# Kernel tuning notes

Hardware: AMD Instinct MI355X
Metric: run time of the kernel (lower is better)

Reference implementation:

```python
import jax, jax.numpy as jnp
import numpy as np

P = 3            # spline degree
N_KNOTS = 68     # len(t); K = N_KNOTS - P - 1 = 64
B, D_IN, D_OUT = 4096, 256, 256


def bspline_basis(u, t, p):
    """Vectorized Cox-de Boor recursion.
    u: (N,) evaluation points; t: (n,) sorted knot vector.
    Returns (N, n - p - 1) basis matrix.
    """
    n = t.shape[0]
    uu = u[:, None]                                   # (N, 1)
    # degree-0 indicators over half-open knot intervals: (N, n-1)
    Bmat = ((uu >= t[None, :-1]) & (uu < t[None, 1:])).astype(u.dtype)
    for d in range(1, p + 1):
        ld = t[d:n - 1] - t[:n - d - 1]               # (n-d-1,) left denominators
        rd = t[d + 1:] - t[1:n - d]                   # (n-d-1,) right denominators
        lt = jnp.where(ld > 0, (uu - t[None, :n - d - 1]) / jnp.where(ld > 0, ld, 1.0), 0.0)
        rt = jnp.where(rd > 0, (t[None, d + 1:] - uu) / jnp.where(rd > 0, rd, 1.0), 0.0)
        Bmat = lt * Bmat[:, :-1] + rt * Bmat[:, 1:]
    return Bmat                                        # (N, K)


def setup_inputs() -> dict:
    key = jax.random.key(0)
    k1, k2 = jax.random.split(key)
    K = N_KNOTS - P - 1
    x = jax.random.normal(k1, (B, D_IN), dtype=jnp.float32)
    coeffs = 0.01 * jax.random.normal(k2, (D_OUT, D_IN, K), dtype=jnp.float32)
    mask = jnp.ones((D_OUT, D_IN), dtype=jnp.float32)
    t = jnp.linspace(-4.0, 4.0, N_KNOTS, dtype=jnp.float32)
    return {"x": x, "coeffs": coeffs, "mask": mask, "t": t}


def reference(x, coeffs, mask, t):
    b, d_in = x.shape
    # basis for all (batch, input-dim) points at once -> (B, d_in, K)
    Bx = bspline_basis(x.reshape(-1), t, P).reshape(b, d_in, -1)
    C = coeffs * mask[..., None]                      # (d_out, d_in, K)
    y = jnp.einsum('bik,oik->bo', Bx, C)              # (B, d_out)
    return y
```

## Files before the change

### kernel.cpp

```cpp
#include <hip/hip_runtime.h>

#define NKNOTS 68
#define B_     4096
#define DIN    256
#define DOUT   256
#define KB_    64
#define BM     128
#define BN     128
#define LDT    72
#define KSPLIT 16
#define IPS    (DIN / KSPLIT)

typedef unsigned short ushort_t;
typedef __bf16 bf16_t;
typedef bf16_t  bf16x8   __attribute__((ext_vector_type(8)));
typedef float   f32x4    __attribute__((ext_vector_type(4)));
typedef unsigned int u32x4 __attribute__((ext_vector_type(4)));
typedef ushort_t us16x4  __attribute__((ext_vector_type(4)));

typedef __attribute__((address_space(1))) const unsigned int gu32;
typedef __attribute__((address_space(3))) unsigned int lu32;

__device__ __forceinline__ float bf2f(ushort_t b) {
    union { unsigned u; float f; } c; c.u = ((unsigned)b) << 16; return c.f;
}
__device__ __forceinline__ ushort_t f2bf(float f) {
    union { float f; unsigned u; } c; c.f = f;
    unsigned u = c.u;
    return (ushort_t)((u + 0x7FFFu + ((u >> 16) & 1u)) >> 16);
}
__device__ __forceinline__ bool is_fp32(const void* tkn) {
    return ((*(const unsigned*)tkn) & 0xFFFFu) == 0u;
}

__global__ void kan_prep(const void* __restrict__ coeffs,
                         const void* __restrict__ mask,
                         const void* __restrict__ x,
                         const void* __restrict__ tkn,
                         ushort_t* __restrict__ cp,
                         ushort_t* __restrict__ basis4,
                         unsigned char* __restrict__ span) {
    __shared__ float tt[NKNOTS];
    int blk = blockIdx.x;
    int lt  = threadIdx.x;
    bool f32 = is_fp32(tkn);

    if (blk < 2048) {
        int tid = blk * 256 + lt;
        int oi = tid >> 3;
        int k8 = (tid & 7) * 8;
        size_t base = (size_t)oi * KB_ + k8;
        float v[8], m;
        if (f32) {
            const float* cf = (const float*)coeffs + base;
            f32x4 a = *(const f32x4*)cf;
            f32x4 b = *(const f32x4*)(cf + 4);
            v[0]=a.x; v[1]=a.y; v[2]=a.z; v[3]=a.w; v[4]=b.x; v[5]=b.y; v[6]=b.z; v[7]=b.w;
            m = ((const float*)mask)[oi];
        } else {
            const ushort_t* ch = (const ushort_t*)coeffs + base;
            u32x4 w = *(const u32x4*)ch;
            const ushort_t* h = (const ushort_t*)&w;
            #pragma unroll
            for (int e = 0; e < 8; ++e) v[e] = bf2f(h[e]);
            m = bf2f(((const ushort_t*)mask)[oi]);
        }
        us16x4 o0v, o1v;
        #pragma unroll
        for (int e = 0; e < 4; ++e) o0v[e] = f2bf(v[e] * m);
        #pragma unroll
        for (int e = 0; e < 4; ++e) o1v[e] = f2bf(v[4 + e] * m);
        *(us16x4*)(cp + base)     = o0v;
        *(us16x4*)(cp + base + 4) = o1v;
    } else {
        if (lt < NKNOTS) tt[lt] = f32 ? ((const float*)tkn)[lt] : bf2f(((const ushort_t*)tkn)[lt]);
        __syncthreads();
        int g = (blk - 2048) * 256 + lt;
        float u = f32 ? ((const float*)x)[g] : bf2f(((const ushort_t*)x)[g]);
        float N0 = 0.f, N1 = 0.f, N2 = 0.f, N3 = 0.f;
        int j = 0;
        bool valid = (u >= tt[0]) && (u < tt[NKNOTS - 1]);
        if (valid) {
            int lo = 0, hi = NKNOTS - 1;
            #pragma unroll
            for (int it = 0; it < 7; ++it) {
                int mid = (lo + hi) >> 1;
                if (u < tt[mid]) hi = mid; else lo = mid;
            }
            j = lo;
            float Nv[4];
            Nv[0] = 1.f; Nv[1] = 0.f; Nv[2] = 0.f; Nv[3] = 0.f;
            #pragma unroll
            for (int d = 1; d <= 3; ++d) {
                float saved = 0.f;
                #pragma unroll
                for (int r = 0; r < 3; ++r) {
                    if (r < d) {
                        int il = j + r + 1 - d;
                        int ir = j + r + 1;
                        il = il < 0 ? 0 : (il > 67 ? 67 : il);
                        ir = ir > 67 ? 67 : ir;
                        float tl = tt[il], tr = tt[ir];
                        float denom = tr - tl;
                        float temp = (denom > 0.f) ? Nv[r] / denom : 0.f;
                        Nv[r] = saved + (tr - u) * temp;
                        saved = (u - tl) * temp;
                    }
                }
                Nv[d] = saved;
            }
            N0 = Nv[0]; N1 = Nv[1]; N2 = Nv[2]; N3 = Nv[3];
        }
        int s = j - 3;
        int sc = s < 0 ? 0 : (s > 60 ? 60 : s);
        us16x4 o4;
        #pragma unroll
        for (int r = 0; r < 4; ++r) {
            int rr = (sc + r) - s;
            float v = 0.f;
            v = (rr == 0) ? N0 : v;
            v = (rr == 1) ? N1 : v;
            v = (rr == 2) ? N2 : v;
            v = (rr == 3) ? N3 : v;
            o4[r] = f2bf(v);
        }
        ((us16x4*)basis4)[g] = o4;
        span[g] = (unsigned char)sc;
    }
}

__global__ __launch_bounds__(256, 4) void kan_gemm(
    const ushort_t* __restrict__ cp,
    const ushort_t* __restrict__ basis4,
    const unsigned char* __restrict__ span,
    ushort_t* __restrict__ part)
{
    __shared__ __align__(16) ushort_t As[BM * LDT];
    __shared__ __align__(16) ushort_t Bs[BM * KB_];

    int t  = threadIdx.x;
    int bx = blockIdx.x;
    int kt = bx & (KSPLIT - 1);
    int mt = (bx >> 4) & 31;
    int nt = bx >> 9;
    int b0 = mt * BM;
    int o0 = nt * BN;
    int i0 = kt * IPS;

    int wave = t >> 6;
    int lane = t & 63;
    int wm = (wave & 1) * 64;
    int wn = (wave >> 1) * 64;
    int l15 = lane & 15;
    int l4  = lane >> 4;

    {
        unsigned* As32 = (unsigned*)As;
        #pragma unroll
        for (int j = 0; j < (BM * LDT / 2) / 256; ++j) As32[t + j * 256] = 0u;
    }
    __syncthreads();

    f32x4 acc[4][4];
    #pragma unroll
    for (int a = 0; a < 4; ++a)
        #pragma unroll
        for (int b = 0; b < 4; ++b)
            acc[a][b] = (f32x4){0.f, 0.f, 0.f, 0.f};

    int zrow = t >> 2;
    int zq   = t & 3;
    int last0 = 0, last1 = 0;

    for (int ii = 0; ii < IPS; ++ii) {
        int i = i0 + ii;
        size_t gi0 = (size_t)(b0 + zrow) * DIN + i;
        size_t gi1 = (size_t)(b0 + zrow + 64) * DIN + i;
        int s0 = span[gi0];
        int s1 = span[gi1];
        ushort_t bv0 = basis4[gi0 * 4 + zq];
        ushort_t bv1 = basis4[gi1 * 4 + zq];
        #pragma unroll
        for (int j = 0; j < 4; ++j) {
            int slot = wave * 256 + j * 64 + lane;
            int row  = slot >> 3;
            int c    = (slot & 7) ^ (row & 7);
            const ushort_t* g = cp + ((size_t)(o0 + row) * DIN + i) * KB_ + c * 8;
            lu32* l = (lu32*)(Bs + (wave * 256 + j * 64) * 8);
            __builtin_amdgcn_global_load_lds((gu32*)g, l, 16, 0, 0);
        }
        As[zrow * LDT + last0 + zq] = 0;
        As[(zrow + 64) * LDT + last1 + zq] = 0;
        As[zrow * LDT + s0 + zq] = bv0;
        As[(zrow + 64) * LDT + s1 + zq] = bv1;
        last0 = s0; last1 = s1;
        __syncthreads();
        #pragma unroll
        for (int ks = 0; ks < 2; ++ks) {
            bf16x8 af[4], bfr[4];
            #pragma unroll
            for (int a = 0; a < 4; ++a)
                af[a] = *(const bf16x8*)(As + (wm + a * 16 + l15) * LDT + ks * 32 + l4 * 8);
            #pragma unroll
            for (int b = 0; b < 4; ++b) {
                int brow = wn + b * 16 + l15;
                int c2 = (ks * 4 + l4) ^ (brow & 7);
                bfr[b] = *(const bf16x8*)(Bs + brow * KB_ + c2 * 8);
            }
            #pragma unroll
            for (int a = 0; a < 4; ++a)
                #pragma unroll
                for (int b = 0; b < 4; ++b)
                    acc[a][b] = __builtin_amdgcn_mfma_f32_16x16x32_bf16(af[a], bfr[b], acc[a][b], 0, 0, 0);
        }
        __syncthreads();
    }
    ushort_t* pout = part + (size_t)kt * (B_ * DOUT);
    #pragma unroll
    for (int a = 0; a < 4; ++a) {
        int row_base = b0 + wm + a * 16 + l4 * 4;
        #pragma unroll
        for (int b = 0; b < 4; ++b) {
            int col = o0 + wn + b * 16 + l15;
            #pragma unroll
            for (int e = 0; e < 4; ++e)
                pout[(size_t)(row_base + e) * DOUT + col] = f2bf(acc[a][b][e]);
        }
    }
}

__global__ void kan_reduce(const ushort_t* __restrict__ part,
                           const void* __restrict__ tkn,
                           void* __restrict__ out) {
    int g = blockIdx.x * 256 + threadIdx.x;
    const us16x4* p4 = (const us16x4*)part;
    f32x4 s = (f32x4){0.f, 0.f, 0.f, 0.f};
    #pragma unroll
    for (int kt = 0; kt < KSPLIT; ++kt) {
        us16x4 v = p4[(size_t)kt * (B_ * DOUT / 4) + g];
        s.x += bf2f(v[0]); s.y += bf2f(v[1]); s.z += bf2f(v[2]); s.w += bf2f(v[3]);
    }
    if (is_fp32(tkn)) {
        ((f32x4*)out)[g] = s;
    } else {
        us16x4 o;
        o[0] = f2bf(s.x); o[1] = f2bf(s.y); o[2] = f2bf(s.z); o[3] = f2bf(s.w);
        ((us16x4*)out)[g] = o;
    }
}

extern "C" void kernel_launch(void* const* d_in, const int* in_sizes, int n_in,
                              void* d_out, int out_size, void* d_ws, size_t ws_size,
                              hipStream_t stream) {
    const void* x      = d_in[0];
    const void* coeffs = d_in[1];
    const void* mask   = d_in[2];
    const void* tkn    = d_in[3];

    char* ws = (char*)d_ws;
    ushort_t* cp            = (ushort_t*)(ws);
    ushort_t* basis4        = (ushort_t*)(ws + (8u  << 20));
    unsigned char* spanbuf  = (unsigned char*)(ws + (16u << 20));
    ushort_t* part          = (ushort_t*)(ws + (17u << 20));

    kan_prep<<<6144, 256, 0, stream>>>(coeffs, mask, x, tkn, cp, basis4, spanbuf);
    kan_gemm<<<1024, 256, 0, stream>>>(cp, basis4, spanbuf, part);
    kan_reduce<<<1024, 256, 0, stream>>>(part, tkn, d_out);
}
```

Measured before the change: 118.6 us.

## Double-buffer coefficient tiles in LDS and prefetch next basis slice

```diff
diff --git a/kernel.cpp b/kernel.cpp
--- a/kernel.cpp
+++ b/kernel.cpp
@@ -129,14 +129,14 @@
     }
 }
 
-__global__ __launch_bounds__(256, 4) void kan_gemm(
+__global__ __launch_bounds__(256, 3) void kan_gemm(
     const ushort_t* __restrict__ cp,
     const ushort_t* __restrict__ basis4,
     const unsigned char* __restrict__ span,
     ushort_t* __restrict__ part)
 {
     __shared__ __align__(16) ushort_t As[BM * LDT];
-    __shared__ __align__(16) ushort_t Bs[BM * KB_];
+    __shared__ __align__(16) ushort_t Bs[2][BM * KB_];
 
     int t  = threadIdx.x;
     int bx = blockIdx.x;
@@ -154,12 +154,31 @@
     int l15 = lane & 15;
     int l4  = lane >> 4;
 
+    int slot0 = wave * 256 + lane;
+    int zrow = t >> 2;
+    int zq   = t & 3;
+
     {
         unsigned* As32 = (unsigned*)As;
         #pragma unroll
         for (int j = 0; j < (BM * LDT / 2) / 256; ++j) As32[t + j * 256] = 0u;
     }
-    __syncthreads();
+
+    #pragma unroll
+    for (int j = 0; j < 4; ++j) {
+        int slot = slot0 + j * 64;
+        int row  = slot >> 3;
+        int c    = (slot & 7) ^ (row & 7);
+        const ushort_t* g = cp + ((size_t)(o0 + row) * DIN + i0) * KB_ + c * 8;
+        lu32* l = (lu32*)(Bs[0] + (wave * 256 + j * 64) * 8);
+        __builtin_amdgcn_global_load_lds((gu32*)g, l, 16, 0, 0);
+    }
+    size_t gi0 = (size_t)(b0 + zrow) * DIN + i0;
+    size_t gi1 = (size_t)(b0 + zrow + 64) * DIN + i0;
+    int cur_s0 = span[gi0];
+    int cur_s1 = span[gi1];
+    ushort_t cur_b0 = basis4[gi0 * 4 + zq];
+    ushort_t cur_b1 = basis4[gi1 * 4 + zq];
 
     f32x4 acc[4][4];
     #pragma unroll
@@ -168,33 +187,35 @@
         for (int b = 0; b < 4; ++b)
             acc[a][b] = (f32x4){0.f, 0.f, 0.f, 0.f};
 
-    int zrow = t >> 2;
-    int zq   = t & 3;
+    __syncthreads();
+
     int last0 = 0, last1 = 0;
-
     for (int ii = 0; ii < IPS; ++ii) {
-        int i = i0 + ii;
-        size_t gi0 = (size_t)(b0 + zrow) * DIN + i;
-        size_t gi1 = (size_t)(b0 + zrow + 64) * DIN + i;
-        int s0 = span[gi0];
-        int s1 = span[gi1];
-        ushort_t bv0 = basis4[gi0 * 4 + zq];
-        ushort_t bv1 = basis4[gi1 * 4 + zq];
-        #pragma unroll
-        for (int j = 0; j < 4; ++j) {
-            int slot = wave * 256 + j * 64 + lane;
-            int row  = slot >> 3;
-            int c    = (slot & 7) ^ (row & 7);
-            const ushort_t* g = cp + ((size_t)(o0 + row) * DIN + i) * KB_ + c * 8;
-            lu32* l = (lu32*)(Bs + (wave * 256 + j * 64) * 8);
-            __builtin_amdgcn_global_load_lds((gu32*)g, l, 16, 0, 0);
-        }
+        int p = ii & 1;
         As[zrow * LDT + last0 + zq] = 0;
         As[(zrow + 64) * LDT + last1 + zq] = 0;
-        As[zrow * LDT + s0 + zq] = bv0;
-        As[(zrow + 64) * LDT + s1 + zq] = bv1;
-        last0 = s0; last1 = s1;
+        As[zrow * LDT + cur_s0 + zq] = cur_b0;
+        As[(zrow + 64) * LDT + cur_s1 + zq] = cur_b1;
+        last0 = cur_s0; last1 = cur_s1;
         __syncthreads();
+        if (ii + 1 < IPS) {
+            int i1 = i0 + ii + 1;
+            #pragma unroll
+            for (int j = 0; j < 4; ++j) {
+                int slot = slot0 + j * 64;
+                int row  = slot >> 3;
+                int c    = (slot & 7) ^ (row & 7);
+                const ushort_t* g = cp + ((size_t)(o0 + row) * DIN + i1) * KB_ + c * 8;
+                lu32* l = (lu32*)(Bs[p ^ 1] + (wave * 256 + j * 64) * 8);
+                __builtin_amdgcn_global_load_lds((gu32*)g, l, 16, 0, 0);
+            }
+            size_t ni0 = (size_t)(b0 + zrow) * DIN + i1;
+            size_t ni1 = (size_t)(b0 + zrow + 64) * DIN + i1;
+            cur_s0 = span[ni0];
+            cur_s1 = span[ni1];
+            cur_b0 = basis4[ni0 * 4 + zq];
+            cur_b1 = basis4[ni1 * 4 + zq];
+        }
         #pragma unroll
         for (int ks = 0; ks < 2; ++ks) {
             bf16x8 af[4], bfr[4];
@@ -205,7 +226,7 @@
             for (int b = 0; b < 4; ++b) {
                 int brow = wn + b * 16 + l15;
                 int c2 = (ks * 4 + l4) ^ (brow & 7);
-                bfr[b] = *(const bf16x8*)(Bs + brow * KB_ + c2 * 8);
+                bfr[b] = *(const bf16x8*)(Bs[p] + brow * KB_ + c2 * 8);
             }
             #pragma unroll
             for (int a = 0; a < 4; ++a)
```

Result: slower. 125.6 us (+5.9%).

## Build sparse basis MFMA fragments in registers and double-buffer coefficient tiles

Applied to the files above, without the earlier changes.

```diff
diff --git a/kernel.cpp b/kernel.cpp
--- a/kernel.cpp
+++ b/kernel.cpp
@@ -7,8 +7,7 @@
 #define KB_    64
 #define BM     128
 #define BN     128
-#define LDT    72
-#define KSPLIT 16
+#define KSPLIT 8
 #define IPS    (DIN / KSPLIT)
 
 typedef unsigned short ushort_t;
@@ -17,6 +16,7 @@
 typedef float   f32x4    __attribute__((ext_vector_type(4)));
 typedef unsigned int u32x4 __attribute__((ext_vector_type(4)));
 typedef ushort_t us16x4  __attribute__((ext_vector_type(4)));
+typedef unsigned long long u64_t;
 
 typedef __attribute__((address_space(1))) const unsigned int gu32;
 typedef __attribute__((address_space(3))) unsigned int lu32;
@@ -38,8 +38,7 @@
                          const void* __restrict__ x,
                          const void* __restrict__ tkn,
                          ushort_t* __restrict__ cp,
-                         ushort_t* __restrict__ basis4,
-                         unsigned char* __restrict__ span) {
+                         u32x4* __restrict__ rec) {
     __shared__ float tt[NKNOTS];
     int blk = blockIdx.x;
     int lt  = threadIdx.x;
@@ -113,7 +112,7 @@
         }
         int s = j - 3;
         int sc = s < 0 ? 0 : (s > 60 ? 60 : s);
-        us16x4 o4;
+        ushort_t hb[4];
         #pragma unroll
         for (int r = 0; r < 4; ++r) {
             int rr = (sc + r) - s;
@@ -122,27 +121,47 @@
             v = (rr == 1) ? N1 : v;
             v = (rr == 2) ? N2 : v;
             v = (rr == 3) ? N3 : v;
-            o4[r] = f2bf(v);
-        }
-        ((us16x4*)basis4)[g] = o4;
-        span[g] = (unsigned char)sc;
-    }
-}
-
-__global__ __launch_bounds__(256, 4) void kan_gemm(
+            hb[r] = f2bf(v);
+        }
+        u32x4 rv;
+        rv.x = ((unsigned)hb[1] << 16) | hb[0];
+        rv.y = ((unsigned)hb[3] << 16) | hb[2];
+        rv.z = (unsigned)sc;
+        rv.w = 0u;
+        rec[g] = rv;
+    }
+}
+
+__device__ __forceinline__ void build_frags(u64_t Bv, int s, int k0,
+                                            bf16x8& af0, bf16x8& af1) {
+    int e0 = s - k0;
+    bool in0 = (unsigned)(e0 + 3)  <= 10u;
+    bool in1 = (unsigned)(e0 - 29) <= 10u;
+    int e = in1 ? (e0 - 32) : e0;
+    int shm = (e << 4) & 63;
+    u64_t l = Bv << shm;
+    u64_t r = (Bv >> 1) >> (63 - shm);
+    u64_t neg = Bv >> (((-e) << 4) & 63);
+    u64_t w0 = (e >= 0) ? ((e <= 3) ? l : 0ull) : neg;
+    u64_t w1 = ((unsigned)(e - 1) <= 2u) ? r : (((unsigned)(e - 4) <= 3u) ? l : 0ull);
+    union U { u64_t q[2]; bf16x8 v; } u0, u1;
+    u0.q[0] = in0 ? w0 : 0ull; u0.q[1] = in0 ? w1 : 0ull;
+    u1.q[0] = in1 ? w0 : 0ull; u1.q[1] = in1 ? w1 : 0ull;
+    af0 = u0.v; af1 = u1.v;
+}
+
+__global__ __launch_bounds__(256, 2) void kan_gemm(
     const ushort_t* __restrict__ cp,
-    const ushort_t* __restrict__ basis4,
-    const unsigned char* __restrict__ span,
+    const u32x4* __restrict__ rec,
     ushort_t* __restrict__ part)
 {
-    __shared__ __align__(16) ushort_t As[BM * LDT];
-    __shared__ __align__(16) ushort_t Bs[BM * KB_];
+    __shared__ __align__(16) ushort_t Bs[2][BN * KB_];
 
     int t  = threadIdx.x;
     int bx = blockIdx.x;
     int kt = bx & (KSPLIT - 1);
-    int mt = (bx >> 4) & 31;
-    int nt = bx >> 9;
+    int mt = (bx >> 3) & 31;
+    int nt = bx >> 8;
     int b0 = mt * BM;
     int o0 = nt * BN;
     int i0 = kt * IPS;
@@ -153,13 +172,30 @@
     int wn = (wave >> 1) * 64;
     int l15 = lane & 15;
     int l4  = lane >> 4;
-
-    {
-        unsigned* As32 = (unsigned*)As;
-        #pragma unroll
-        for (int j = 0; j < (BM * LDT / 2) / 256; ++j) As32[t + j * 256] = 0u;
-    }
-    __syncthreads();
+    int k0  = l4 * 8;
+
+    #define STAGE(i_, p_)                                                              \
+        {                                                                              \
+            _Pragma("unroll")                                                          \
+            for (int j = 0; j < 4; ++j) {                                              \
+                int slot = wave * 256 + j * 64 + lane;                                 \
+                int row  = slot >> 3;                                                  \
+                int c    = (slot & 7) ^ (row & 7);                                     \
+                const ushort_t* g = cp + ((size_t)(o0 + row) * DIN + (i_)) * KB_ + c * 8; \
+                lu32* l = (lu32*)(&Bs[p_][(wave * 256 + j * 64) * 8]);                 \
+                __builtin_amdgcn_global_load_lds((gu32*)g, l, 16, 0, 0);               \
+            }                                                                          \
+        }
+
+    size_t ridx[4];
+    #pragma unroll
+    for (int a = 0; a < 4; ++a)
+        ridx[a] = (size_t)(b0 + wm + a * 16 + l15) * DIN + i0;
+
+    STAGE(i0, 0);
+    u32x4 rcur[4], rnext[4];
+    #pragma unroll
+    for (int a = 0; a < 4; ++a) rcur[a] = rec[ridx[a]];
 
     f32x4 acc[4][4];
     #pragma unroll
@@ -168,53 +204,42 @@
         for (int b = 0; b < 4; ++b)
             acc[a][b] = (f32x4){0.f, 0.f, 0.f, 0.f};
 
-    int zrow = t >> 2;
-    int zq   = t & 3;
-    int last0 = 0, last1 = 0;
+    __syncthreads();
 
     for (int ii = 0; ii < IPS; ++ii) {
-        int i = i0 + ii;
-        size_t gi0 = (size_t)(b0 + zrow) * DIN + i;
-        size_t gi1 = (size_t)(b0 + zrow + 64) * DIN + i;
-        int s0 = span[gi0];
-        int s1 = span[gi1];
-        ushort_t bv0 = basis4[gi0 * 4 + zq];
-        ushort_t bv1 = basis4[gi1 * 4 + zq];
-        #pragma unroll
-        for (int j = 0; j < 4; ++j) {
-            int slot = wave * 256 + j * 64 + lane;
-            int row  = slot >> 3;
-            int c    = (slot & 7) ^ (row & 7);
-            const ushort_t* g = cp + ((size_t)(o0 + row) * DIN + i) * KB_ + c * 8;
-            lu32* l = (lu32*)(Bs + (wave * 256 + j * 64) * 8);
-            __builtin_amdgcn_global_load_lds((gu32*)g, l, 16, 0, 0);
-        }
-        As[zrow * LDT + last0 + zq] = 0;
-        As[(zrow + 64) * LDT + last1 + zq] = 0;
-        As[zrow * LDT + s0 + zq] = bv0;
-        As[(zrow + 64) * LDT + s1 + zq] = bv1;
-        last0 = s0; last1 = s1;
-        __syncthreads();
-        #pragma unroll
-        for (int ks = 0; ks < 2; ++ks) {
-            bf16x8 af[4], bfr[4];
-            #pragma unroll
-            for (int a = 0; a < 4; ++a)
-                af[a] = *(const bf16x8*)(As + (wm + a * 16 + l15) * LDT + ks * 32 + l4 * 8);
+        int p = ii & 1;
+        if (ii + 1 < IPS) {
+            STAGE(i0 + ii + 1, p ^ 1);
+            #pragma unroll
+            for (int a = 0; a < 4; ++a) rnext[a] = rec[ridx[a] + ii + 1];
+        }
+        bf16x8 bfr[2][4];
+        #pragma unroll
+        for (int ks = 0; ks < 2; ++ks)
             #pragma unroll
             for (int b = 0; b < 4; ++b) {
                 int brow = wn + b * 16 + l15;
                 int c2 = (ks * 4 + l4) ^ (brow & 7);
-                bfr[b] = *(const bf16x8*)(Bs + brow * KB_ + c2 * 8);
+                bfr[ks][b] = *(const bf16x8*)(&Bs[p][brow * KB_ + c2 * 8]);
             }
-            #pragma unroll
-            for (int a = 0; a < 4; ++a)
-                #pragma unroll
-                for (int b = 0; b < 4; ++b)
-                    acc[a][b] = __builtin_amdgcn_mfma_f32_16x16x32_bf16(af[a], bfr[b], acc[a][b], 0, 0, 0);
-        }
+        #pragma unroll
+        for (int a = 0; a < 4; ++a) {
+            u64_t Bv = ((u64_t)rcur[a].y << 32) | rcur[a].x;
+            int s = (int)rcur[a].z;
+            bf16x8 af0, af1;
+            build_frags(Bv, s, k0, af0, af1);
+            #pragma unroll
+            for (int b = 0; b < 4; ++b)
+                acc[a][b] = __builtin_amdgcn_mfma_f32_16x16x32_bf16(af0, bfr[0][b], acc[a][b], 0, 0, 0);
+            #pragma unroll
+            for (int b = 0; b < 4; ++b)
+                acc[a][b] = __builtin_amdgcn_mfma_f32_16x16x32_bf16(af1, bfr[1][b], acc[a][b], 0, 0, 0);
+        }
+        #pragma unroll
+        for (int a = 0; a < 4; ++a) rcur[a] = rnext[a];
         __syncthreads();
     }
+
     ushort_t* pout = part + (size_t)kt * (B_ * DOUT);
     #pragma unroll
     for (int a = 0; a < 4; ++a) {
@@ -227,6 +252,7 @@
                 pout[(size_t)(row_base + e) * DOUT + col] = f2bf(acc[a][b][e]);
         }
     }
+    #undef STAGE
 }
 
 __global__ void kan_reduce(const ushort_t* __restrict__ part,
@@ -258,12 +284,11 @@
     const void* tkn    = d_in[3];
 
     char* ws = (char*)d_ws;
-    ushort_t* cp            = (ushort_t*)(ws);
-    ushort_t* basis4        = (ushort_t*)(ws + (8u  << 20));
-    unsigned char* spanbuf  = (unsigned char*)(ws + (16u << 20));
-    ushort_t* part          = (ushort_t*)(ws + (17u << 20));
-
-    kan_prep<<<6144, 256, 0, stream>>>(coeffs, mask, x, tkn, cp, basis4, spanbuf);
-    kan_gemm<<<1024, 256, 0, stream>>>(cp, basis4, spanbuf, part);
+    ushort_t* cp   = (ushort_t*)(ws);
+    u32x4*    rec  = (u32x4*)(ws + (8u  << 20));
+    ushort_t* part = (ushort_t*)(ws + (24u << 20));
+
+    kan_prep<<<6144, 256, 0, stream>>>(coeffs, mask, x, tkn, cp, rec);
+    kan_gemm<<<512, 256, 0, stream>>>(cp, rec, part);
     kan_reduce<<<1024, 256, 0, stream>>>(part, tkn, d_out);
 }
```

Result: slower. 133.8 us (+12.8%).

## Double-buffer GEMM LDS tiles and split K across waves in 512-thread blocks

Applied to the files above, without the earlier changes.

```diff
diff --git a/kernel.cpp b/kernel.cpp
--- a/kernel.cpp
+++ b/kernel.cpp
@@ -8,8 +8,9 @@
 #define BM     128
 #define BN     128
 #define LDT    72
-#define KSPLIT 16
+#define KSPLIT 8
 #define IPS    (DIN / KSPLIT)
+#define KPART  (KSPLIT * 2)
 
 typedef unsigned short ushort_t;
 typedef __bf16 bf16_t;
@@ -129,37 +130,63 @@
     }
 }
 
-__global__ __launch_bounds__(256, 4) void kan_gemm(
+__global__ __launch_bounds__(512, 4) void kan_gemm(
     const ushort_t* __restrict__ cp,
     const ushort_t* __restrict__ basis4,
     const unsigned char* __restrict__ span,
     ushort_t* __restrict__ part)
 {
-    __shared__ __align__(16) ushort_t As[BM * LDT];
-    __shared__ __align__(16) ushort_t Bs[BM * KB_];
+    __shared__ __align__(16) ushort_t As[2][BM * LDT];
+    __shared__ __align__(16) ushort_t Bs[2][BN * KB_];
 
     int t  = threadIdx.x;
     int bx = blockIdx.x;
-    int kt = bx & (KSPLIT - 1);
-    int mt = (bx >> 4) & 31;
-    int nt = bx >> 9;
+    int kt = bx & 7;
+    int mt = (bx >> 3) & 31;
+    int nt = bx >> 8;
     int b0 = mt * BM;
     int o0 = nt * BN;
     int i0 = kt * IPS;
 
     int wave = t >> 6;
     int lane = t & 63;
-    int wm = (wave & 1) * 64;
-    int wn = (wave >> 1) * 64;
+    int wm  = (wave & 1) * 64;
+    int wn  = ((wave >> 1) & 1) * 64;
+    int ksw = wave >> 2;
+    int kofs = ksw * 32;
     int l15 = lane & 15;
     int l4  = lane >> 4;
 
+    #define STAGE(i_, p_)                                                                 \
+        {                                                                                 \
+            _Pragma("unroll")                                                             \
+            for (int j = 0; j < 2; ++j) {                                                 \
+                int slot = wave * 128 + j * 64 + lane;                                    \
+                int row  = slot >> 3;                                                     \
+                int c    = (slot & 7) ^ (row & 7);                                        \
+                const ushort_t* g = cp + ((size_t)(o0 + row) * DIN + (i_)) * KB_ + c * 8; \
+                lu32* l = (lu32*)(&Bs[p_][(wave * 128 + j * 64) * 8]);                    \
+                __builtin_amdgcn_global_load_lds((gu32*)g, l, 16, 0, 0);                  \
+            }                                                                             \
+        }
+
     {
         unsigned* As32 = (unsigned*)As;
         #pragma unroll
-        for (int j = 0; j < (BM * LDT / 2) / 256; ++j) As32[t + j * 256] = 0u;
-    }
-    __syncthreads();
+        for (int j = 0; j < (2 * BM * LDT / 2) / 512; ++j) As32[t + j * 512] = 0u;
+    }
+
+    int zrow = t >> 2;
+    int zq   = t & 3;
+    size_t gbase = (size_t)(b0 + zrow) * DIN;
+
+    STAGE(i0, 0);
+    int cur_s = span[gbase + i0];
+    ushort_t cur_b = basis4[(gbase + i0) * 4 + zq];
+    int nxt_s = span[gbase + i0 + 1];
+    ushort_t nxt_b = basis4[(gbase + i0 + 1) * 4 + zq];
+    int pre_s = 0; ushort_t pre_b = 0;
+    int lastw[2] = {0, 0};
 
     f32x4 acc[4][4];
     #pragma unroll
@@ -168,54 +195,48 @@
         for (int b = 0; b < 4; ++b)
             acc[a][b] = (f32x4){0.f, 0.f, 0.f, 0.f};
 
-    int zrow = t >> 2;
-    int zq   = t & 3;
-    int last0 = 0, last1 = 0;
-
-    for (int ii = 0; ii < IPS; ++ii) {
-        int i = i0 + ii;
-        size_t gi0 = (size_t)(b0 + zrow) * DIN + i;
-        size_t gi1 = (size_t)(b0 + zrow + 64) * DIN + i;
-        int s0 = span[gi0];
-        int s1 = span[gi1];
-        ushort_t bv0 = basis4[gi0 * 4 + zq];
-        ushort_t bv1 = basis4[gi1 * 4 + zq];
-        #pragma unroll
-        for (int j = 0; j < 4; ++j) {
-            int slot = wave * 256 + j * 64 + lane;
-            int row  = slot >> 3;
-            int c    = (slot & 7) ^ (row & 7);
-            const ushort_t* g = cp + ((size_t)(o0 + row) * DIN + i) * KB_ + c * 8;
-            lu32* l = (lu32*)(Bs + (wave * 256 + j * 64) * 8);
-            __builtin_amdgcn_global_load_lds((gu32*)g, l, 16, 0, 0);
-        }
-        As[zrow * LDT + last0 + zq] = 0;
-        As[(zrow + 64) * LDT + last1 + zq] = 0;
-        As[zrow * LDT + s0 + zq] = bv0;
-        As[(zrow + 64) * LDT + s1 + zq] = bv1;
-        last0 = s0; last1 = s1;
-        __syncthreads();
-        #pragma unroll
-        for (int ks = 0; ks < 2; ++ks) {
-            bf16x8 af[4], bfr[4];
-            #pragma unroll
-            for (int a = 0; a < 4; ++a)
-                af[a] = *(const bf16x8*)(As + (wm + a * 16 + l15) * LDT + ks * 32 + l4 * 8);
-            #pragma unroll
-            for (int b = 0; b < 4; ++b) {
-                int brow = wn + b * 16 + l15;
-                int c2 = (ks * 4 + l4) ^ (brow & 7);
-                bfr[b] = *(const bf16x8*)(Bs + brow * KB_ + c2 * 8);
-            }
-            #pragma unroll
-            for (int a = 0; a < 4; ++a)
-                #pragma unroll
-                for (int b = 0; b < 4; ++b)
-                    acc[a][b] = __builtin_amdgcn_mfma_f32_16x16x32_bf16(af[a], bfr[b], acc[a][b], 0, 0, 0);
-        }
-        __syncthreads();
-    }
-    ushort_t* pout = part + (size_t)kt * (B_ * DOUT);
+    __syncthreads();
+    As[0][zrow * LDT + cur_s + zq] = cur_b;
+    lastw[0] = cur_s;
+    __syncthreads();
+
+    #define BODY(ii_, p_)                                                                  \
+        {                                                                                  \
+            if ((ii_) + 1 < IPS) {                                                         \
+                STAGE(i0 + (ii_) + 1, (p_) ^ 1);                                           \
+                      \
+                As[(p_) ^ 1][zrow * LDT + lastw[(p_) ^ 1] + zq] = 0;                       \
+                As[(p_) ^ 1][zrow * LDT + nxt_s + zq] = nxt_b;                             \
+                lastw[(p_) ^ 1] = nxt_s;                                                   \
+                int i2 = i0 + (((ii_) + 2 < IPS) ? (ii_) + 2 : (ii_) + 1);                 \
+                pre_s = span[gbase + i2];                                                  \
+                pre_b = basis4[(gbase + i2) * 4 + zq];                                     \
+            }                                                                              \
+            bf16x8 af[4], bfr[4];                                                          \
+            _Pragma("unroll")                                                              \
+            for (int a = 0; a < 4; ++a)                                                    \
+                af[a] = *(const bf16x8*)(&As[p_][(wm + a * 16 + l15) * LDT + kofs + l4 * 8]); \
+            _Pragma("unroll")                                                              \
+            for (int b = 0; b < 4; ++b) {                                                  \
+                int brow = wn + b * 16 + l15;                                              \
+                int c2 = (ksw * 4 + l4) ^ (brow & 7);                                      \
+                bfr[b] = *(const bf16x8*)(&Bs[p_][brow * KB_ + c2 * 8]);                   \
+            }                                                                              \
+            _Pragma("unroll")                                                              \
+            for (int a = 0; a < 4; ++a)                                                    \
+                _Pragma("unroll")                                                          \
+                for (int b = 0; b < 4; ++b)                                                \
+                    acc[a][b] = __builtin_amdgcn_mfma_f32_16x16x32_bf16(af[a], bfr[b], acc[a][b], 0, 0, 0); \
+            nxt_s = pre_s; nxt_b = pre_b;                                                  \
+            __syncthreads();                                                               \
+        }
+
+    for (int jj = 0; jj < IPS; jj += 2) {
+        BODY(jj, 0);
+        BODY(jj + 1, 1);
+    }
+
+    ushort_t* pout = part + (size_t)(kt * 2 + ksw) * (B_ * DOUT);
     #pragma unroll
     for (int a = 0; a < 4; ++a) {
         int row_base = b0 + wm + a * 16 + l4 * 4;
@@ -227,6 +248,8 @@
                 pout[(size_t)(row_base + e) * DOUT + col] = f2bf(acc[a][b][e]);
         }
     }
+    #undef BODY
+    #undef STAGE
 }
 
 __global__ void kan_reduce(const ushort_t* __restrict__ part,
@@ -236,7 +259,7 @@
     const us16x4* p4 = (const us16x4*)part;
     f32x4 s = (f32x4){0.f, 0.f, 0.f, 0.f};
     #pragma unroll
-    for (int kt = 0; kt < KSPLIT; ++kt) {
+    for (int kt = 0; kt < KPART; ++kt) {
         us16x4 v = p4[(size_t)kt * (B_ * DOUT / 4) + g];
         s.x += bf2f(v[0]); s.y += bf2f(v[1]); s.z += bf2f(v[2]); s.w += bf2f(v[3]);
     }
@@ -264,6 +287,6 @@
     ushort_t* part          = (ushort_t*)(ws + (17u << 20));
 
     kan_prep<<<6144, 256, 0, stream>>>(coeffs, mask, x, tkn, cp, basis4, spanbuf);
-    kan_gemm<<<1024, 256, 0, stream>>>(cp, basis4, spanbuf, part);
+    kan_gemm<<<512, 512, 0, stream>>>(cp, basis4, spanbuf, part);
     kan_reduce<<<1024, 256, 0, stream>>>(part, tkn, d_out);
 }
```

After: 126.5 us. +6.6%, slower.
